# Performance work log

Measured on AMD Instinct MI355X. Metric: run time of the kernel, lower is better.

The kernel has to match this reference:

```python
import jax, jax.numpy as jnp
import numpy as np

B, S, H, NCOL, NH = 32, 512, 768, 32, 12
HD = H // NH  # head dim 64
LN_EPS = 1e-12


def setup_inputs() -> dict:
    key = jax.random.key(0)
    ks = jax.random.split(key, 20)
    s = 0.02
    inp = {
        'hidden_states': jax.random.normal(ks[0], (B, S, H), jnp.float32),
        'column_embeddings': jax.random.normal(ks[1], (B, NCOL, H), jnp.float32),
        'column_categories': jax.random.randint(ks[2], (B, NCOL), 0, 2, jnp.int32),
        'value_mask': jax.random.randint(ks[3], (B, S), 0, NCOL + 1, jnp.int32),
        'Wd': jax.random.normal(ks[4], (H, H), jnp.float32) * s,
        'bd': jnp.zeros((H,), jnp.float32),
        'Wc': jax.random.normal(ks[5], (H, H), jnp.float32) * s,
        'bc': jnp.zeros((H,), jnp.float32),
        'Wq': jax.random.normal(ks[6], (H, H), jnp.float32) * s,
        'bq': jnp.zeros((H,), jnp.float32),
        'Wk': jax.random.normal(ks[7], (H, H), jnp.float32) * s,
        'bk': jnp.zeros((H,), jnp.float32),
        'Wv': jax.random.normal(ks[8], (H, H), jnp.float32) * s,
        'bv': jnp.zeros((H,), jnp.float32),
        'Wo': jax.random.normal(ks[9], (H, H), jnp.float32) * s,
        'bo': jnp.zeros((H,), jnp.float32),
        'ln_g': jnp.ones((H,), jnp.float32),
        'ln_b': jnp.zeros((H,), jnp.float32),
    }
    return inp


def _layernorm(x, g, b):
    mu = jnp.mean(x, axis=-1, keepdims=True)
    var = jnp.mean(jnp.square(x - mu), axis=-1, keepdims=True)
    return (x - mu) * jax.lax.rsqrt(var + LN_EPS) * g + b


def reference(hidden_states, column_embeddings, column_categories, value_mask,
              Wd, bd, Wc, bc, Wq, bq, Wk, bk, Wv, bv, Wo, bo, ln_g, ln_b):
    # dense branch
    h_ = hidden_states @ Wd.T + bd  # [B,S,H]
    # column gather: zero out category==0 columns, prepend zero row for index 0
    table = column_embeddings * (column_categories == 1)[..., None].astype(column_embeddings.dtype)
    table = jnp.concatenate([jnp.zeros_like(table[:, :1]), table], axis=1)  # [B,NCOL+1,H]
    h_col = jnp.take_along_axis(table, value_mask[..., None].astype(jnp.int32), axis=1)  # [B,S,H]
    h = jax.nn.gelu(h_ + (h_col @ Wc.T + bc), approximate=False)
    # Roberta self-attention
    def heads(x):
        return x.reshape(B, S, NH, HD).transpose(0, 2, 1, 3)  # [B,NH,S,HD]
    q = heads(h @ Wq.T + bq)
    k = heads(h @ Wk.T + bk)
    v = heads(h @ Wv.T + bv)
    scores = jnp.einsum('bhsd,bhtd->bhst', q, k) / jnp.sqrt(jnp.float32(HD))
    probs = jax.nn.softmax(scores, axis=-1)
    ctx = jnp.einsum('bhst,bhtd->bhsd', probs, v).transpose(0, 2, 1, 3).reshape(B, S, H)
    # self-output: dense + residual + layernorm
    out = _layernorm(ctx @ Wo.T + bo + h, ln_g, ln_b)
    return out
```

## Files before the change

kernel.cpp:

```cpp
#include <hip/hip_runtime.h>
#include <hip/hip_bf16.h>
#include <math.h>
#include <stdint.h>

#define B_    32
#define S_    512
#define H_    768
#define NH_   12
#define HD_   64
#define NCOL_ 32
#define M_    (B_*S_)

typedef __bf16 bf16;
typedef __bf16 bf16x8 __attribute__((ext_vector_type(8)));
typedef __bf16 bf16x4 __attribute__((ext_vector_type(4)));
typedef float  f32x4  __attribute__((ext_vector_type(4)));

__device__ __forceinline__ void async_load16(const void* g, void* l) {
    __builtin_amdgcn_global_load_lds(
        (__attribute__((address_space(1))) unsigned int*)g,
        (__attribute__((address_space(3))) unsigned int*)l, 16, 0, 0);
}

__device__ __forceinline__ bf16x8 cvt8(const float* p) {
    const float4* fp = (const float4*)p;
    float4 x = fp[0], y = fp[1];
    bf16x8 r;
    r[0] = (bf16)x.x; r[1] = (bf16)x.y; r[2] = (bf16)x.z; r[3] = (bf16)x.w;
    r[4] = (bf16)y.x; r[5] = (bf16)y.y; r[6] = (bf16)y.z; r[7] = (bf16)y.w;
    return r;
}

__global__ __launch_bounds__(256) void cvt_kernel(
    const float* __restrict__ hidden, const float* __restrict__ ce,
    const int* __restrict__ cc, const int* __restrict__ vm,
    const float* __restrict__ Wd, const float* __restrict__ Wc,
    const float* __restrict__ Wq, const float* __restrict__ Wk,
    const float* __restrict__ Wv, const float* __restrict__ Wo,
    const float* __restrict__ bq, const float* __restrict__ bk,
    const float* __restrict__ bv,
    bf16* __restrict__ hbf, bf16* __restrict__ hcol,
    bf16* __restrict__ wpack, float* __restrict__ bqkv)
{
    int blk = blockIdx.x;
    if (blk < 6144) {
        int id = blk * 256 + threadIdx.x;
        int row = id / 96, c = id - row * 96;
        *(bf16x8*)&hbf[(long)row * H_ + c * 8] = cvt8(hidden + (long)row * H_ + c * 8);
    } else if (blk < 12288) {
        int id = (blk - 6144) * 256 + threadIdx.x;
        int row = id / 96, c = id - row * 96;
        int b = row >> 9;
        int m = vm[row];
        bf16x8 val;
#pragma unroll
        for (int i = 0; i < 8; i++) val[i] = (bf16)0.0f;
        if (m > 0) {
            int col = m - 1;
            if (cc[b * NCOL_ + col] == 1)
                val = cvt8(ce + ((long)(b * NCOL_ + col)) * H_ + c * 8);
        }
        *(bf16x8*)&hcol[(long)row * H_ + c * 8] = val;
    } else {
        int id = (blk - 12288) * 256 + threadIdx.x;
        if (id < 442368) {
            const float* src;
            int r = id;
            if      (r < 73728)  { src = Wd; }
            else if (r < 147456) { src = Wc; r -= 73728; }
            else if (r < 221184) { src = Wq; r -= 147456; }
            else if (r < 294912) { src = Wk; r -= 221184; }
            else if (r < 368640) { src = Wv; r -= 294912; }
            else                 { src = Wo; r -= 368640; }
            *(bf16x8*)&wpack[(long)id * 8] = cvt8(src + (long)r * 8);
        } else if (id < 442656) {
            int j0 = (id - 442368) * 8;
#pragma unroll
            for (int i = 0; i < 8; i++) {
                int j = j0 + i;
                float v = (j < 768) ? bq[j] : (j < 1536) ? bk[j - 768] : bv[j - 1536];
                bqkv[j] = v;
            }
        }
    }
}

template<int MODE>
__global__ __launch_bounds__(256) void gemm_bt(
    const bf16* __restrict__ A0, const bf16* __restrict__ A1,
    const bf16* __restrict__ B0, const bf16* __restrict__ B1,
    const float* __restrict__ bias1, const float* __restrict__ bias2,
    const bf16* __restrict__ resid, bf16* __restrict__ out,
    int K, int KSPLIT)
{
    __shared__ __align__(16) bf16 As[2][128 * 32];
    __shared__ __align__(16) bf16 Bs[2][128 * 32];

    const int tid  = threadIdx.x;
    const int lane = tid & 63;
    const int wave = tid >> 6;
    const int wm   = wave & 1;
    const int wn   = wave >> 1;
    const int m0   = blockIdx.x * 128;
    const int n0   = blockIdx.y * 128;

    const int srow = tid >> 2;
    const int scol = (tid & 3) * 8;

    f32x4 acc[4][4];
    const f32x4 zero4 = {0.f, 0.f, 0.f, 0.f};
#pragma unroll
    for (int i = 0; i < 4; i++)
#pragma unroll
        for (int j = 0; j < 4; j++) acc[i][j] = zero4;

    const int a_off = (wm * 64 + (lane & 15)) * 32 + (lane >> 4) * 8;
    const int b_off = (wn * 64 + (lane & 15)) * 32 + (lane >> 4) * 8;

    auto stage = [&](int kk, int buf) {
        const bf16* ag = (kk < KSPLIT) ? A0 + kk : A1 + (kk - KSPLIT);
        const bf16* bg = (kk < KSPLIT) ? B0 + kk : B1 + (kk - KSPLIT);
        async_load16(ag + (long)(m0 + srow) * H_ + scol,      &As[buf][tid * 8]);
        async_load16(ag + (long)(m0 + 64 + srow) * H_ + scol, &As[buf][2048 + tid * 8]);
        async_load16(bg + (long)(n0 + srow) * H_ + scol,      &Bs[buf][tid * 8]);
        async_load16(bg + (long)(n0 + 64 + srow) * H_ + scol, &Bs[buf][2048 + tid * 8]);
    };

    stage(0, 0);
    int cur = 0;
    for (int k0 = 0; k0 < K; k0 += 32, cur ^= 1) {
        __syncthreads();
        if (k0 + 32 < K) stage(k0 + 32, cur ^ 1);

        bf16x8 af[4], bfr[4];
#pragma unroll
        for (int i = 0; i < 4; i++) af[i]  = *(const bf16x8*)(&As[cur][a_off + i * 512]);
#pragma unroll
        for (int j = 0; j < 4; j++) bfr[j] = *(const bf16x8*)(&Bs[cur][b_off + j * 512]);
#pragma unroll
        for (int i = 0; i < 4; i++)
#pragma unroll
            for (int j = 0; j < 4; j++)
                acc[i][j] = __builtin_amdgcn_mfma_f32_16x16x32_bf16(af[i], bfr[j], acc[i][j], 0, 0, 0);
    }

    const int c_r = (lane >> 4) * 4;
    const int c_c = lane & 15;

    int sec = 0;
    if (MODE == 1) sec = (n0 >= 1536) ? 2 : ((n0 >= 768) ? 1 : 0);
    bf16* dst = (MODE == 1) ? out + (long)sec * M_ * H_ : out;

#pragma unroll
    for (int j = 0; j < 4; j++) {
        const int col = n0 + wn * 64 + j * 16 + c_c;
        float bias = bias1[col];
        if (MODE == 0) bias += bias2[col];
#pragma unroll
        for (int i = 0; i < 4; i++) {
            if (MODE == 1 && sec == 2) {
                const int row0 = m0 + wm * 64 + i * 16 + c_r;
                int b = row0 >> 9, s = row0 & 511;
                int cs = col - 1536;
                int head = cs >> 6, d = cs & 63;
                bf16x4 pk;
#pragma unroll
                for (int r = 0; r < 4; r++) pk[r] = (bf16)(acc[i][j][r] + bias);
                *(bf16x4*)&dst[(((long)(b * NH_ + head)) * HD_ + d) * S_ + s] = pk;
            } else {
#pragma unroll
                for (int r = 0; r < 4; r++) {
                    const int row = m0 + wm * 64 + i * 16 + c_r + r;
                    float v = acc[i][j][r] + bias;
                    if (MODE == 0) {
                        v = 0.5f * v * (1.0f + erff(v * 0.70710678118654752f));
                        dst[(long)row * H_ + col] = (bf16)v;
                    } else if (MODE == 1) {
                        int b = row >> 9, s = row & 511;
                        int cs = col - sec * 768;
                        int head = cs >> 6, d = cs & 63;
                        dst[(((long)(b * NH_ + head)) * S_ + s) * HD_ + d] = (bf16)v;
                    } else {
                        v += (float)resid[(long)row * H_ + col];
                        dst[(long)row * H_ + col] = (bf16)v;
                    }
                }
            }
        }
    }
}

#define QP 72

__global__ __launch_bounds__(256) void attn_kernel(
    const bf16* __restrict__ q, const bf16* __restrict__ k,
    const bf16* __restrict__ vt, bf16* __restrict__ ctx)
{
    __shared__ __align__(16) bf16 Qs[64 * QP];
    __shared__ __align__(16) bf16 Ks[64 * QP];
    __shared__ __align__(16) bf16 Vt[64 * QP];
    __shared__ __align__(16) bf16 Ps[4][16 * QP];

    const int tid  = threadIdx.x;
    const int lane = tid & 63;
    const int w    = tid >> 6;
    const int quad = lane >> 4;
    const int ln16 = lane & 15;

    const int bid = blockIdx.x;
    const int qt  = bid / 384;
    const int g   = bid - qt * 384;
    const int b   = g / 12;
    const int h   = g - b * 12;
    const long base = ((long)(b * NH_ + h)) * S_ * HD_;

    const int r0 = tid >> 2;
    const int e0 = (tid & 3) * 16;

    {
        const bf16* qg = q + base + (long)qt * 64 * HD_;
        *(uint4*)&Qs[r0 * QP + e0]     = *(const uint4*)&qg[r0 * HD_ + e0];
        *(uint4*)&Qs[r0 * QP + e0 + 8] = *(const uint4*)&qg[r0 * HD_ + e0 + 8];
    }
    const bf16* kg = k  + base;
    const bf16* vg = vt + base;
    uint4 kr0 = *(const uint4*)&kg[r0 * HD_ + e0];
    uint4 kr1 = *(const uint4*)&kg[r0 * HD_ + e0 + 8];
    uint4 vr0 = *(const uint4*)&vg[(long)r0 * S_ + e0];
    uint4 vr1 = *(const uint4*)&vg[(long)r0 * S_ + e0 + 8];
    __syncthreads();

    const bf16x8 bq0 = *(const bf16x8*)&Qs[(w * 16 + ln16) * QP + quad * 8];
    const bf16x8 bq1 = *(const bf16x8*)&Qs[(w * 16 + ln16) * QP + 32 + quad * 8];

    f32x4 O[4];
    const f32x4 zero4 = {0.f, 0.f, 0.f, 0.f};
#pragma unroll
    for (int t = 0; t < 4; t++) O[t] = zero4;
    float mo = -1e30f, l = 0.f;

    for (int kc = 0; kc < 8; kc++) {
        __syncthreads();
        *(uint4*)&Ks[r0 * QP + e0]     = kr0;
        *(uint4*)&Ks[r0 * QP + e0 + 8] = kr1;
        *(uint4*)&Vt[r0 * QP + e0]     = vr0;
        *(uint4*)&Vt[r0 * QP + e0 + 8] = vr1;
        {
            int kcn = (kc < 7) ? kc + 1 : 7;
            kr0 = *(const uint4*)&kg[(long)kcn * 64 * HD_ + r0 * HD_ + e0];
            kr1 = *(const uint4*)&kg[(long)kcn * 64 * HD_ + r0 * HD_ + e0 + 8];
            vr0 = *(const uint4*)&vg[(long)r0 * S_ + kcn * 64 + e0];
            vr1 = *(const uint4*)&vg[(long)r0 * S_ + kcn * 64 + e0 + 8];
        }
        __syncthreads();

        f32x4 sc[4];
#pragma unroll
        for (int i = 0; i < 4; i++) {
            bf16x8 a0 = *(const bf16x8*)&Ks[(i * 16 + ln16) * QP + quad * 8];
            bf16x8 a1 = *(const bf16x8*)&Ks[(i * 16 + ln16) * QP + 32 + quad * 8];
            sc[i] = zero4;
            sc[i] = __builtin_amdgcn_mfma_f32_16x16x32_bf16(a0, bq0, sc[i], 0, 0, 0);
            sc[i] = __builtin_amdgcn_mfma_f32_16x16x32_bf16(a1, bq1, sc[i], 0, 0, 0);
        }

        float cm = -1e30f;
#pragma unroll
        for (int i = 0; i < 4; i++)
#pragma unroll
            for (int r = 0; r < 4; r++) {
                float s = sc[i][r] * 0.125f;
                sc[i][r] = s;
                cm = fmaxf(cm, s);
            }
        cm = fmaxf(cm, __shfl_xor(cm, 16));
        cm = fmaxf(cm, __shfl_xor(cm, 32));
        float mn = fmaxf(mo, cm);
        float alpha = __expf(mo - mn);
        float rs = 0.f;
#pragma unroll
        for (int i = 0; i < 4; i++) {
            bf16x4 pk;
#pragma unroll
            for (int r = 0; r < 4; r++) {
                float p = __expf(sc[i][r] - mn);
                rs += p;
                pk[r] = (bf16)p;
            }
            *(bf16x4*)&Ps[w][ln16 * QP + i * 16 + quad * 4] = pk;
        }
        rs += __shfl_xor(rs, 16);
        rs += __shfl_xor(rs, 32);
        l  = l * alpha + rs;
        mo = mn;
#pragma unroll
        for (int t = 0; t < 4; t++)
#pragma unroll
            for (int r = 0; r < 4; r++) O[t][r] *= alpha;

        bf16x8 bp0 = *(const bf16x8*)&Ps[w][ln16 * QP + quad * 8];
        bf16x8 bp1 = *(const bf16x8*)&Ps[w][ln16 * QP + 32 + quad * 8];
#pragma unroll
        for (int dt = 0; dt < 4; dt++) {
            bf16x8 a0 = *(const bf16x8*)&Vt[(dt * 16 + ln16) * QP + quad * 8];
            bf16x8 a1 = *(const bf16x8*)&Vt[(dt * 16 + ln16) * QP + 32 + quad * 8];
            O[dt] = __builtin_amdgcn_mfma_f32_16x16x32_bf16(a0, bp0, O[dt], 0, 0, 0);
            O[dt] = __builtin_amdgcn_mfma_f32_16x16x32_bf16(a1, bp1, O[dt], 0, 0, 0);
        }
    }

    {
        float inv = 1.0f / l;
#pragma unroll
        for (int dt = 0; dt < 4; dt++) {
            bf16x4 ov;
#pragma unroll
            for (int r = 0; r < 4; r++) ov[r] = (bf16)(O[dt][r] * inv);
            *(bf16x4*)&Qs[(w * 16 + ln16) * QP + dt * 16 + quad * 4] = ov;
        }
    }
    __syncthreads();
    {
        uint4 o0 = *(const uint4*)&Qs[r0 * QP + e0];
        uint4 o1 = *(const uint4*)&Qs[r0 * QP + e0 + 8];
        bf16* cg = ctx + ((long)(b * S_ + qt * 64 + r0)) * H_ + h * HD_;
        *(uint4*)&cg[e0]     = o0;
        *(uint4*)&cg[e0 + 8] = o1;
    }
}

__global__ __launch_bounds__(256) void ln_kernel(
    const bf16* __restrict__ y, const float* __restrict__ g,
    const float* __restrict__ be, float* __restrict__ out)
{
    const int lane = threadIdx.x & 63;
    const int w    = threadIdx.x >> 6;
    const long row = (long)blockIdx.x * 4 + w;
    const bf16* yr = y + row * H_;

    float x[12];
    float sum = 0.f, ss = 0.f;
#pragma unroll
    for (int j = 0; j < 12; j++) {
        x[j] = (float)yr[j * 64 + lane];
        sum += x[j];
        ss  += x[j] * x[j];
    }
#pragma unroll
    for (int m = 1; m < 64; m <<= 1) {
        sum += __shfl_xor(sum, m);
        ss  += __shfl_xor(ss, m);
    }
    const float mu  = sum * (1.0f / 768.0f);
    float var = ss * (1.0f / 768.0f) - mu * mu;
    const float rs = rsqrtf(fmaxf(var, 0.f) + 1e-12f);
#pragma unroll
    for (int j = 0; j < 12; j++) {
        int c = j * 64 + lane;
        out[row * H_ + c] = (x[j] - mu) * rs * g[c] + be[c];
    }
}

extern "C" void kernel_launch(void* const* d_in, const int* in_sizes, int n_in,
                              void* d_out, int out_size, void* d_ws, size_t ws_size,
                              hipStream_t stream)
{
    const float* hidden = (const float*)d_in[0];
    const float* ce     = (const float*)d_in[1];
    const int*   cc     = (const int*)d_in[2];
    const int*   vm     = (const int*)d_in[3];
    const float* Wd     = (const float*)d_in[4];
    const float* bd     = (const float*)d_in[5];
    const float* Wc     = (const float*)d_in[6];
    const float* bc     = (const float*)d_in[7];
    const float* Wq     = (const float*)d_in[8];
    const float* bq     = (const float*)d_in[9];
    const float* Wk     = (const float*)d_in[10];
    const float* bk     = (const float*)d_in[11];
    const float* Wv     = (const float*)d_in[12];
    const float* bv     = (const float*)d_in[13];
    const float* Wo     = (const float*)d_in[14];
    const float* bo     = (const float*)d_in[15];
    const float* lng    = (const float*)d_in[16];
    const float* lnb    = (const float*)d_in[17];

    const long NE = (long)M_ * H_;
    bf16* ws   = (bf16*)d_ws;
    bf16* hbuf = ws;
    bf16* qkv  = ws + NE;
    bf16* hbf  = qkv;
    bf16* hcol = qkv + NE;
    bf16* qb   = qkv;
    bf16* kb   = qkv + NE;
    bf16* vb   = qkv + 2 * NE;
    bf16* wpack = ws + 4 * NE;
    const bf16* Wd_b  = wpack;
    const bf16* Wc_b  = wpack + 589824;
    const bf16* Wq_b  = wpack + 1179648;
    const bf16* Wk_b  = wpack + 1769472;
    const bf16* Wv_b  = wpack + 2359296;
    const bf16* Wo_b  = wpack + 2949120;
    float* bqkv = (float*)(wpack + 3538944);
    bf16* ctx = (bf16*)d_out;

    cvt_kernel<<<14018, 256, 0, stream>>>(hidden, ce, cc, vm, Wd, Wc, Wq, Wk, Wv, Wo,
                                          bq, bk, bv, hbf, hcol, wpack, bqkv);

    dim3 g6(M_ / 128, 6);
    dim3 g18(M_ / 128, 18);
    gemm_bt<0><<<g6, 256, 0, stream>>>(hbf, hcol, Wd_b, Wc_b, bd, bc, nullptr, hbuf, 2 * H_, H_);
    gemm_bt<1><<<g18, 256, 0, stream>>>(hbuf, hbuf, Wq_b, Wq_b, bqkv, nullptr, nullptr, qkv, H_, 3 * H_);
    attn_kernel<<<3072, 256, 0, stream>>>(qb, kb, vb, ctx);
    gemm_bt<2><<<g6, 256, 0, stream>>>(ctx, ctx, Wo_b, Wo_b, bo, nullptr, hbuf, hbuf, H_, H_);
    ln_kernel<<<M_ / 4, 256, 0, stream>>>(hbuf, lng, lnb, (float*)d_out);
}
```

Measured before the change: 395.2 us.

## Restructure GEMM into 256x128 tiles with triple-buffered swizzled LDS pipeline

Rewrites the shared GEMM kernel to use 512 threads with 256x128 output tiles, K-step of 64, and a three-stage LDS ring buffer. LDS rows are XOR-swizzled to avoid bank conflicts, and global loads for tile t+2 are split across two compute phases. Explicit waitcnt, sched_barrier and s_setprio calls order MFMA work against the async loads. The change raises LDS use (about 144KB) and register pressure, and halves the block count, which risks lower occupancy.

```diff
diff --git a/kernel.cpp b/kernel.cpp
--- a/kernel.cpp
+++ b/kernel.cpp
@@ -86,26 +86,47 @@
 }
 
 template<int MODE>
-__global__ __launch_bounds__(256) void gemm_bt(
+__global__ __launch_bounds__(512) void gemm_bt(
     const bf16* __restrict__ A0, const bf16* __restrict__ A1,
     const bf16* __restrict__ B0, const bf16* __restrict__ B1,
     const float* __restrict__ bias1, const float* __restrict__ bias2,
     const bf16* __restrict__ resid, bf16* __restrict__ out,
     int K, int KSPLIT)
 {
-    __shared__ __align__(16) bf16 As[2][128 * 32];
-    __shared__ __align__(16) bf16 Bs[2][128 * 32];
+    __shared__ __align__(16) bf16 SA[3][256 * 64];
+    __shared__ __align__(16) bf16 SB[3][128 * 64];
 
     const int tid  = threadIdx.x;
     const int lane = tid & 63;
     const int wave = tid >> 6;
-    const int wm   = wave & 1;
-    const int wn   = wave >> 1;
-    const int m0   = blockIdx.x * 128;
+    const int wr   = wave >> 1;
+    const int wc   = wave & 1;
+    const int quad = lane >> 4;
+    const int ln16 = lane & 15;
+    const int rsw  = ln16 & 7;
+    const int m0   = blockIdx.x * 256;
     const int n0   = blockIdx.y * 128;
 
-    const int srow = tid >> 2;
-    const int scol = (tid & 3) * 8;
+    int arow[4], acol[4];
+#pragma unroll
+    for (int q = 0; q < 4; q++) {
+        int row = (q * 512 + tid) >> 3;
+        arow[q] = row;
+        acol[q] = ((tid & 7) ^ (row & 7)) * 8;
+    }
+
+    auto stageA = [&](int kt, int bsel, int q) {
+        int kk = kt * 64;
+        const bf16* ag = (kk < KSPLIT) ? A0 + kk : A1 + (kk - KSPLIT);
+        async_load16(ag + (long)(m0 + arow[q]) * H_ + acol[q],
+                     &SA[bsel][(q * 512 + tid) * 8]);
+    };
+    auto stageB = [&](int kt, int bsel, int q) {
+        int kk = kt * 64;
+        const bf16* bg = (kk < KSPLIT) ? B0 + kk : B1 + (kk - KSPLIT);
+        async_load16(bg + (long)(n0 + arow[q]) * H_ + acol[q],
+                     &SB[bsel][(q * 512 + tid) * 8]);
+    };
 
     f32x4 acc[4][4];
     const f32x4 zero4 = {0.f, 0.f, 0.f, 0.f};
@@ -114,38 +135,87 @@
 #pragma unroll
         for (int j = 0; j < 4; j++) acc[i][j] = zero4;
 
-    const int a_off = (wm * 64 + (lane & 15)) * 32 + (lane >> 4) * 8;
-    const int b_off = (wn * 64 + (lane & 15)) * 32 + (lane >> 4) * 8;
-
-    auto stage = [&](int kk, int buf) {
-        const bf16* ag = (kk < KSPLIT) ? A0 + kk : A1 + (kk - KSPLIT);
-        const bf16* bg = (kk < KSPLIT) ? B0 + kk : B1 + (kk - KSPLIT);
-        async_load16(ag + (long)(m0 + srow) * H_ + scol,      &As[buf][tid * 8]);
-        async_load16(ag + (long)(m0 + 64 + srow) * H_ + scol, &As[buf][2048 + tid * 8]);
-        async_load16(bg + (long)(n0 + srow) * H_ + scol,      &Bs[buf][tid * 8]);
-        async_load16(bg + (long)(n0 + 64 + srow) * H_ + scol, &Bs[buf][2048 + tid * 8]);
-    };
-
-    stage(0, 0);
-    int cur = 0;
-    for (int k0 = 0; k0 < K; k0 += 32, cur ^= 1) {
-        __syncthreads();
-        if (k0 + 32 < K) stage(k0 + 32, cur ^ 1);
-
-        bf16x8 af[4], bfr[4];
-#pragma unroll
-        for (int i = 0; i < 4; i++) af[i]  = *(const bf16x8*)(&As[cur][a_off + i * 512]);
-#pragma unroll
-        for (int j = 0; j < 4; j++) bfr[j] = *(const bf16x8*)(&Bs[cur][b_off + j * 512]);
+    int aoff[4][2], boff[4][2];
+#pragma unroll
+    for (int i = 0; i < 4; i++)
+#pragma unroll
+        for (int ks = 0; ks < 2; ks++) {
+            int ch = (((ks << 2) | quad) ^ rsw) * 8;
+            aoff[i][ks] = (wr * 64 + i * 16 + ln16) * 64 + ch;
+            boff[i][ks] = (wc * 64 + i * 16 + ln16) * 64 + ch;
+        }
+
+    const int nt = K >> 6;
+
+#pragma unroll
+    for (int q = 0; q < 4; q++) stageA(0, 0, q);
+    stageB(0, 0, 0); stageB(0, 0, 1);
+#pragma unroll
+    for (int q = 0; q < 4; q++) stageA(1, 1, q);
+    stageB(1, 1, 0); stageB(1, 1, 1);
+    asm volatile("s_waitcnt vmcnt(6)" ::: "memory");
+    __builtin_amdgcn_sched_barrier(0);
+    __builtin_amdgcn_s_barrier();
+
+    int bs = 0;
+    for (int t = 0; t < nt; ++t) {
+        const bool pf = (t + 2) < nt;
+        const int  ps = (bs + 2 >= 3) ? bs - 1 : bs + 2;
+
+        bf16x8 af[4][2], bfr[4][2];
 #pragma unroll
         for (int i = 0; i < 4; i++)
 #pragma unroll
-            for (int j = 0; j < 4; j++)
-                acc[i][j] = __builtin_amdgcn_mfma_f32_16x16x32_bf16(af[i], bfr[j], acc[i][j], 0, 0, 0);
-    }
-
-    const int c_r = (lane >> 4) * 4;
-    const int c_c = lane & 15;
+            for (int ks = 0; ks < 2; ks++)
+                af[i][ks] = *(const bf16x8*)&SA[bs][aoff[i][ks]];
+#pragma unroll
+        for (int j = 0; j < 2; j++)
+#pragma unroll
+            for (int ks = 0; ks < 2; ks++)
+                bfr[j][ks] = *(const bf16x8*)&SB[bs][boff[j][ks]];
+        if (pf) { stageA(t + 2, ps, 0); stageA(t + 2, ps, 1); stageA(t + 2, ps, 2); }
+        __builtin_amdgcn_s_barrier();
+        asm volatile("s_waitcnt lgkmcnt(0)" ::: "memory");
+        __builtin_amdgcn_sched_barrier(0);
+        __builtin_amdgcn_s_setprio(1);
+#pragma unroll
+        for (int i = 0; i < 4; i++)
+#pragma unroll
+            for (int j = 0; j < 2; j++)
+#pragma unroll
+                for (int ks = 0; ks < 2; ks++)
+                    acc[i][j] = __builtin_amdgcn_mfma_f32_16x16x32_bf16(af[i][ks], bfr[j][ks], acc[i][j], 0, 0, 0);
+        __builtin_amdgcn_s_setprio(0);
+        __builtin_amdgcn_s_barrier();
+
+#pragma unroll
+        for (int j = 2; j < 4; j++)
+#pragma unroll
+            for (int ks = 0; ks < 2; ks++)
+                bfr[j][ks] = *(const bf16x8*)&SB[bs][boff[j][ks]];
+        if (pf) { stageA(t + 2, ps, 3); stageB(t + 2, ps, 0); stageB(t + 2, ps, 1); }
+        __builtin_amdgcn_s_barrier();
+        asm volatile("s_waitcnt lgkmcnt(0)" ::: "memory");
+        __builtin_amdgcn_sched_barrier(0);
+        __builtin_amdgcn_s_setprio(1);
+#pragma unroll
+        for (int i = 0; i < 4; i++)
+#pragma unroll
+            for (int j = 2; j < 4; j++)
+#pragma unroll
+                for (int ks = 0; ks < 2; ks++)
+                    acc[i][j] = __builtin_amdgcn_mfma_f32_16x16x32_bf16(af[i][ks], bfr[j][ks], acc[i][j], 0, 0, 0);
+        __builtin_amdgcn_s_setprio(0);
+
+        if (pf)               { asm volatile("s_waitcnt vmcnt(6)" ::: "memory"); }
+        else if (t + 1 < nt)  { asm volatile("s_waitcnt vmcnt(0)" ::: "memory"); }
+        __builtin_amdgcn_sched_barrier(0);
+        __builtin_amdgcn_s_barrier();
+        bs = (bs + 1 == 3) ? 0 : bs + 1;
+    }
+
+    const int c_r = quad * 4;
+    const int c_c = ln16;
 
     int sec = 0;
     if (MODE == 1) sec = (n0 >= 1536) ? 2 : ((n0 >= 768) ? 1 : 0);
@@ -153,13 +223,13 @@
 
 #pragma unroll
     for (int j = 0; j < 4; j++) {
-        const int col = n0 + wn * 64 + j * 16 + c_c;
+        const int col = n0 + wc * 64 + j * 16 + c_c;
         float bias = bias1[col];
         if (MODE == 0) bias += bias2[col];
 #pragma unroll
         for (int i = 0; i < 4; i++) {
             if (MODE == 1 && sec == 2) {
-                const int row0 = m0 + wm * 64 + i * 16 + c_r;
+                const int row0 = m0 + wr * 64 + i * 16 + c_r;
                 int b = row0 >> 9, s = row0 & 511;
                 int cs = col - 1536;
                 int head = cs >> 6, d = cs & 63;
@@ -170,7 +240,7 @@
             } else {
 #pragma unroll
                 for (int r = 0; r < 4; r++) {
-                    const int row = m0 + wm * 64 + i * 16 + c_r + r;
+                    const int row = m0 + wr * 64 + i * 16 + c_r + r;
                     float v = acc[i][j][r] + bias;
                     if (MODE == 0) {
                         v = 0.5f * v * (1.0f + erff(v * 0.70710678118654752f));
@@ -406,11 +476,11 @@
     cvt_kernel<<<14018, 256, 0, stream>>>(hidden, ce, cc, vm, Wd, Wc, Wq, Wk, Wv, Wo,
                                           bq, bk, bv, hbf, hcol, wpack, bqkv);
 
-    dim3 g6(M_ / 128, 6);
-    dim3 g18(M_ / 128, 18);
-    gemm_bt<0><<<g6, 256, 0, stream>>>(hbf, hcol, Wd_b, Wc_b, bd, bc, nullptr, hbuf, 2 * H_, H_);
-    gemm_bt<1><<<g18, 256, 0, stream>>>(hbuf, hbuf, Wq_b, Wq_b, bqkv, nullptr, nullptr, qkv, H_, 3 * H_);
+    dim3 g6(M_ / 256, 6);
+    dim3 g18(M_ / 256, 18);
+    gemm_bt<0><<<g6, 512, 0, stream>>>(hbf, hcol, Wd_b, Wc_b, bd, bc, nullptr, hbuf, 2 * H_, H_);
+    gemm_bt<1><<<g18, 512, 0, stream>>>(hbuf, hbuf, Wq_b, Wq_b, bqkv, nullptr, nullptr, qkv, H_, 3 * H_);
     attn_kernel<<<3072, 256, 0, stream>>>(qb, kb, vb, ctx);
-    gemm_bt<2><<<g6, 256, 0, stream>>>(ctx, ctx, Wo_b, Wo_b, bo, nullptr, hbuf, hbuf, H_, H_);
+    gemm_bt<2><<<g6, 512, 0, stream>>>(ctx, ctx, Wo_b, Wo_b, bo, nullptr, hbuf, hbuf, H_, H_);
     ln_kernel<<<M_ / 4, 256, 0, stream>>>(hbuf, lng, lnb, (float*)d_out);
 }
```

Measured after the change: 402.7 us. About the same (+1.9%).

## Restructure GEMM: 256x128 tiles, 8 waves, triple-buffered LDS with XOR swizzle

Applied to the files above, without the earlier changes.

The bf16 GEMM kernel now uses 512-thread blocks covering 256x128 output tiles, with the B tile shared by twice as many rows. Double buffering becomes a three-stage async-to-LDS pipeline, two tiles deep, using explicit vmcnt waits and a single barrier per k-step. LDS rows get an XOR swizzle to cut bank conflicts on the fragment reads, and MFMA issue priority is raised with s_setprio. The aim is to hide global-load latency and reduce LDS conflicts and per-tile B traffic, at the cost of more LDS per block (72KB) and possibly lower occupancy or a worse tail with half as many blocks.

```diff
diff --git a/kernel.cpp b/kernel.cpp
--- a/kernel.cpp
+++ b/kernel.cpp
@@ -86,26 +86,45 @@
 }
 
 template<int MODE>
-__global__ __launch_bounds__(256) void gemm_bt(
+__global__ __launch_bounds__(512, 4) void gemm_bt(
     const bf16* __restrict__ A0, const bf16* __restrict__ A1,
     const bf16* __restrict__ B0, const bf16* __restrict__ B1,
     const float* __restrict__ bias1, const float* __restrict__ bias2,
     const bf16* __restrict__ resid, bf16* __restrict__ out,
     int K, int KSPLIT)
 {
-    __shared__ __align__(16) bf16 As[2][128 * 32];
-    __shared__ __align__(16) bf16 Bs[2][128 * 32];
+    __shared__ __align__(16) bf16 SA[3][256 * 32];
+    __shared__ __align__(16) bf16 SB[3][128 * 32];
 
     const int tid  = threadIdx.x;
     const int lane = tid & 63;
     const int wave = tid >> 6;
-    const int wm   = wave & 1;
-    const int wn   = wave >> 1;
-    const int m0   = blockIdx.x * 128;
+    const int wr   = wave >> 1;
+    const int wc   = wave & 1;
+    const int quad = lane >> 4;
+    const int ln16 = lane & 15;
+    const int m0   = blockIdx.x * 256;
     const int n0   = blockIdx.y * 128;
 
-    const int srow = tid >> 2;
-    const int scol = (tid & 3) * 8;
+    int arow[2], acol[2];
+#pragma unroll
+    for (int q = 0; q < 2; q++) {
+        int l = q * 512 + tid;
+        int row = l >> 2;
+        arow[q] = row;
+        acol[q] = ((l & 3) ^ ((row >> 1) & 3)) * 8;
+    }
+    const int brow = tid >> 2;
+    const int bcol = ((tid & 3) ^ ((brow >> 1) & 3)) * 8;
+
+    auto stage = [&](int kt, int bsel) {
+        int kk = kt * 32;
+        const bf16* ag = (kk < KSPLIT) ? A0 + kk : A1 + (kk - KSPLIT);
+        const bf16* bg = (kk < KSPLIT) ? B0 + kk : B1 + (kk - KSPLIT);
+        async_load16(ag + (long)(m0 + arow[0]) * H_ + acol[0], &SA[bsel][tid * 8]);
+        async_load16(ag + (long)(m0 + arow[1]) * H_ + acol[1], &SA[bsel][4096 + tid * 8]);
+        async_load16(bg + (long)(n0 + brow)    * H_ + bcol,    &SB[bsel][tid * 8]);
+    };
 
     f32x4 acc[4][4];
     const f32x4 zero4 = {0.f, 0.f, 0.f, 0.f};
@@ -114,38 +133,50 @@
 #pragma unroll
         for (int j = 0; j < 4; j++) acc[i][j] = zero4;
 
-    const int a_off = (wm * 64 + (lane & 15)) * 32 + (lane >> 4) * 8;
-    const int b_off = (wn * 64 + (lane & 15)) * 32 + (lane >> 4) * 8;
-
-    auto stage = [&](int kk, int buf) {
-        const bf16* ag = (kk < KSPLIT) ? A0 + kk : A1 + (kk - KSPLIT);
-        const bf16* bg = (kk < KSPLIT) ? B0 + kk : B1 + (kk - KSPLIT);
-        async_load16(ag + (long)(m0 + srow) * H_ + scol,      &As[buf][tid * 8]);
-        async_load16(ag + (long)(m0 + 64 + srow) * H_ + scol, &As[buf][2048 + tid * 8]);
-        async_load16(bg + (long)(n0 + srow) * H_ + scol,      &Bs[buf][tid * 8]);
-        async_load16(bg + (long)(n0 + 64 + srow) * H_ + scol, &Bs[buf][2048 + tid * 8]);
-    };
+    const int s4 = (ln16 >> 1) & 3;
+    int aoff[4], boff[4];
+#pragma unroll
+    for (int i = 0; i < 4; i++) {
+        aoff[i] = (wr * 64 + i * 16 + ln16) * 32 + (quad ^ s4) * 8;
+        boff[i] = (wc * 64 + i * 16 + ln16) * 32 + (quad ^ s4) * 8;
+    }
+
+    const int nt = K >> 5;
 
     stage(0, 0);
-    int cur = 0;
-    for (int k0 = 0; k0 < K; k0 += 32, cur ^= 1) {
-        __syncthreads();
-        if (k0 + 32 < K) stage(k0 + 32, cur ^ 1);
+    stage(1, 1);
+    asm volatile("s_waitcnt vmcnt(3)" ::: "memory");
+    __builtin_amdgcn_sched_barrier(0);
+    __builtin_amdgcn_s_barrier();
+
+    int bs = 0;
+    for (int t = 0; t < nt; ++t) {
+        const int ps = (bs + 2 >= 3) ? bs - 1 : bs + 2;
 
         bf16x8 af[4], bfr[4];
 #pragma unroll
-        for (int i = 0; i < 4; i++) af[i]  = *(const bf16x8*)(&As[cur][a_off + i * 512]);
-#pragma unroll
-        for (int j = 0; j < 4; j++) bfr[j] = *(const bf16x8*)(&Bs[cur][b_off + j * 512]);
+        for (int i = 0; i < 4; i++) af[i]  = *(const bf16x8*)&SA[bs][aoff[i]];
+#pragma unroll
+        for (int j = 0; j < 4; j++) bfr[j] = *(const bf16x8*)&SB[bs][boff[j]];
+        if (t + 2 < nt) stage(t + 2, ps);
+
+        __builtin_amdgcn_s_setprio(1);
 #pragma unroll
         for (int i = 0; i < 4; i++)
 #pragma unroll
             for (int j = 0; j < 4; j++)
                 acc[i][j] = __builtin_amdgcn_mfma_f32_16x16x32_bf16(af[i], bfr[j], acc[i][j], 0, 0, 0);
-    }
-
-    const int c_r = (lane >> 4) * 4;
-    const int c_c = lane & 15;
+        __builtin_amdgcn_s_setprio(0);
+
+        if (t + 2 < nt)       { asm volatile("s_waitcnt vmcnt(3)" ::: "memory"); }
+        else if (t + 1 < nt)  { asm volatile("s_waitcnt vmcnt(0)" ::: "memory"); }
+        __builtin_amdgcn_sched_barrier(0);
+        if (t + 1 < nt) __builtin_amdgcn_s_barrier();
+        bs = (bs + 1 == 3) ? 0 : bs + 1;
+    }
+
+    const int c_r = quad * 4;
+    const int c_c = ln16;
 
     int sec = 0;
     if (MODE == 1) sec = (n0 >= 1536) ? 2 : ((n0 >= 768) ? 1 : 0);
@@ -153,13 +184,13 @@
 
 #pragma unroll
     for (int j = 0; j < 4; j++) {
-        const int col = n0 + wn * 64 + j * 16 + c_c;
+        const int col = n0 + wc * 64 + j * 16 + c_c;
         float bias = bias1[col];
         if (MODE == 0) bias += bias2[col];
 #pragma unroll
         for (int i = 0; i < 4; i++) {
             if (MODE == 1 && sec == 2) {
-                const int row0 = m0 + wm * 64 + i * 16 + c_r;
+                const int row0 = m0 + wr * 64 + i * 16 + c_r;
                 int b = row0 >> 9, s = row0 & 511;
                 int cs = col - 1536;
                 int head = cs >> 6, d = cs & 63;
@@ -170,7 +201,7 @@
             } else {
 #pragma unroll
                 for (int r = 0; r < 4; r++) {
-                    const int row = m0 + wm * 64 + i * 16 + c_r + r;
+                    const int row = m0 + wr * 64 + i * 16 + c_r + r;
                     float v = acc[i][j][r] + bias;
                     if (MODE == 0) {
                         v = 0.5f * v * (1.0f + erff(v * 0.70710678118654752f));
@@ -406,11 +437,11 @@
     cvt_kernel<<<14018, 256, 0, stream>>>(hidden, ce, cc, vm, Wd, Wc, Wq, Wk, Wv, Wo,
                                           bq, bk, bv, hbf, hcol, wpack, bqkv);
 
-    dim3 g6(M_ / 128, 6);
-    dim3 g18(M_ / 128, 18);
-    gemm_bt<0><<<g6, 256, 0, stream>>>(hbf, hcol, Wd_b, Wc_b, bd, bc, nullptr, hbuf, 2 * H_, H_);
-    gemm_bt<1><<<g18, 256, 0, stream>>>(hbuf, hbuf, Wq_b, Wq_b, bqkv, nullptr, nullptr, qkv, H_, 3 * H_);
+    dim3 g6(M_ / 256, 6);
+    dim3 g18(M_ / 256, 18);
+    gemm_bt<0><<<g6, 512, 0, stream>>>(hbf, hcol, Wd_b, Wc_b, bd, bc, nullptr, hbuf, 2 * H_, H_);
+    gemm_bt<1><<<g18, 512, 0, stream>>>(hbuf, hbuf, Wq_b, Wq_b, bqkv, nullptr, nullptr, qkv, H_, 3 * H_);
     attn_kernel<<<3072, 256, 0, stream>>>(qb, kb, vb, ctx);
-    gemm_bt<2><<<g6, 256, 0, stream>>>(ctx, ctx, Wo_b, Wo_b, bo, nullptr, hbuf, hbuf, H_, H_);
+    gemm_bt<2><<<g6, 512, 0, stream>>>(ctx, ctx, Wo_b, Wo_b, bo, nullptr, hbuf, hbuf, H_, H_);
     ln_kernel<<<M_ / 4, 256, 0, stream>>>(hbuf, lng, lnb, (float*)d_out);
 }
```

Measured after the change: 373.3 us. 1.06x faster.
